# Kernel optimization log

Measured on AMD Instinct MI355X. Metric: run time of the kernel, lower is better.

## Reference

```python
import jax, jax.numpy as jnp
import numpy as np

C = 512
GROUPS = 32
EPS = 1e-5  # torch GroupNorm default


def setup_inputs() -> dict:
    key = jax.random.key(0)
    ks = jax.random.split(key, 11)
    B, H, W = 4, 64, 64
    s = 1.0 / np.sqrt(C)
    inp = {
        "x": jax.random.normal(ks[0], (B, C, H, W), dtype=jnp.float32),
        "gn_scale": jnp.ones((C,), jnp.float32),
        "gn_bias": jnp.zeros((C,), jnp.float32),
        "wq": jax.random.normal(ks[1], (C, C), jnp.float32) * s,
        "bq": jax.random.normal(ks[2], (C,), jnp.float32) * 0.01,
        "wk": jax.random.normal(ks[3], (C, C), jnp.float32) * s,
        "bk": jax.random.normal(ks[4], (C,), jnp.float32) * 0.01,
        "wv": jax.random.normal(ks[5], (C, C), jnp.float32) * s,
        "bv": jax.random.normal(ks[6], (C,), jnp.float32) * 0.01,
        "wo": jax.random.normal(ks[7], (C, C), jnp.float32) * s,
        "bo": jax.random.normal(ks[8], (C,), jnp.float32) * 0.01,
    }
    return inp


def group_norm(x, scale, bias):
    # x: [B, C, H, W]; normalize within each of GROUPS channel groups over (C/G, H, W)
    B, Cc, H, W = x.shape
    xg = x.reshape(B, GROUPS, Cc // GROUPS, H, W)
    mean = jnp.mean(xg, axis=(2, 3, 4), keepdims=True)
    var = jnp.var(xg, axis=(2, 3, 4), keepdims=True)
    xg = (xg - mean) * jax.lax.rsqrt(var + EPS)
    xn = xg.reshape(B, Cc, H, W)
    return xn * scale[None, :, None, None] + bias[None, :, None, None]


def reference(x, gn_scale, gn_bias, wq, bq, wk, bk, wv, bv, wo, bo):
    B, Cc, H, W = x.shape
    h = group_norm(x, gn_scale, gn_bias)
    # 1x1 convs == channel matmuls; work in [B, HW, C] layout
    hf = h.reshape(B, Cc, H * W).transpose(0, 2, 1)  # [B, N, C]
    q = hf @ wq.T + bq                               # [B, N, C]
    k = hf @ wk.T + bk
    v = hf @ wv.T + bv
    scale = jnp.asarray(Cc, x.dtype) ** -0.5
    attn = jnp.einsum("bnc,bmc->bnm", q, k) * scale  # [B, N, N]
    attn = jax.nn.softmax(attn, axis=-1)
    o = jnp.einsum("bnm,bmc->bnc", attn, v)          # [B, N, C]
    o = o @ wo.T + bo
    o = o.transpose(0, 2, 1).reshape(B, Cc, H, W)
    return x + o
```

## Files before the change

kernel.cpp:

```cpp
#include <hip/hip_runtime.h>
#include <cstdint>
#include <cstddef>

typedef unsigned short ushort_t;
typedef __attribute__((ext_vector_type(8))) __bf16 bf16x8;
typedef __attribute__((ext_vector_type(4))) float f32x4;

#define DEVINL __device__ __forceinline__

DEVINL ushort_t f2bf(float f) {
  union { __bf16 b; ushort_t u; } v;
  v.b = (__bf16)f;
  return v.u;
}
DEVINL float bf2f(ushort_t u) {
  union { unsigned u; float f; } v; v.u = ((unsigned)u) << 16;
  return v.f;
}

DEVINL float wred_sum(float x) {
#pragma unroll
  for (int o = 32; o > 0; o >>= 1) x += __shfl_xor(x, o, 64);
  return x;
}

DEVINL void async16(ushort_t* lds, const ushort_t* g) {
  __builtin_amdgcn_global_load_lds(
      (__attribute__((address_space(1))) const unsigned int*)g,
      (__attribute__((address_space(3))) unsigned int*)lds, 16, 0, 0);
}

template <int CPR>
DEVINL int fswz(int r) {
  if constexpr (CPR == 4) return (r >> 2) & 3;
  else return r & 7;
}

__global__ __launch_bounds__(256) void gn_stats_k(const float* __restrict__ x,
                                                  float* __restrict__ stats) {
  const int bg = blockIdx.x;
  const float4* base = (const float4*)(x + ((size_t)bg << 16));
  float s = 0.f, q = 0.f;
  for (int i = threadIdx.x; i < 16384; i += 256) {
    float4 f = base[i];
    s += f.x + f.y + f.z + f.w;
    q += f.x * f.x + f.y * f.y + f.z * f.z + f.w * f.w;
  }
  s = wred_sum(s);
  q = wred_sum(q);
  __shared__ float rs[4], rq[4];
  const int lane = threadIdx.x & 63, wid = threadIdx.x >> 6;
  if (lane == 0) { rs[wid] = s; rq[wid] = q; }
  __syncthreads();
  if (threadIdx.x == 0) {
    float S = rs[0] + rs[1] + rs[2] + rs[3];
    float Q = rq[0] + rq[1] + rq[2] + rq[3];
    float mean = S * (1.f / 65536.f);
    float var = Q * (1.f / 65536.f) - mean * mean;
    stats[2 * bg] = mean;
    stats[2 * bg + 1] = rsqrtf(var + 1e-5f);
  }
}

__global__ __launch_bounds__(256) void gn_apply_k(const float* __restrict__ x,
                                                  const float* __restrict__ stats,
                                                  const float* __restrict__ gs,
                                                  const float* __restrict__ gb,
                                                  ushort_t* __restrict__ h) {
  __shared__ ushort_t tile[32][33];
  const int bid = blockIdx.x;
  const int b = bid >> 11;
  const int r = bid & 2047;
  const int ct = r >> 7, nt = r & 127;
  const int c0 = ct << 5, n0 = nt << 5;
  const int tx = threadIdx.x & 31, ty = threadIdx.x >> 5;
#pragma unroll
  for (int i = 0; i < 4; ++i) {
    const int c = c0 + ty + i * 8;
    const float mean = stats[2 * (b * 32 + (c >> 4))];
    const float rstd = stats[2 * (b * 32 + (c >> 4)) + 1];
    const float xv = x[(((size_t)b * 512 + c) << 12) + n0 + tx];
    tile[ty + i * 8][tx] = f2bf((xv - mean) * rstd * gs[c] + gb[c]);
  }
  __syncthreads();
#pragma unroll
  for (int i = 0; i < 4; ++i) {
    const int n = n0 + ty + i * 8;
    h[(((size_t)b << 12) + n) * 512 + c0 + tx] = tile[tx][ty + i * 8];
  }
}

struct Ptr4 { const float* src[4]; float wsc[4]; };
__global__ __launch_bounds__(256) void cvt_all_k(Ptr4 s, ushort_t* __restrict__ dst) {
  const int i = blockIdx.x * 256 + threadIdx.x;
  const int m = i >> 18;
  dst[i] = f2bf(s.src[m][i & 262143] * s.wsc[m]);
}

struct Ptr3 { const float* bias[3]; ushort_t* out[3]; float bs[3]; };

template <int BM, int BN, int BK, int EPI>
__global__ __launch_bounds__(256) void gemm_nt_k(
    const ushort_t* __restrict__ A, int lda, const ushort_t* __restrict__ Bm, int ldb,
    void* __restrict__ Cout, int ldc, const float* __restrict__ bias,
    const float* __restrict__ resid, float scale, int K,
    size_t azs, size_t bzs, size_t czs, Ptr3 p3) {
  constexpr int CPR = BK / 8;
  constexpr int WTM = BM / 2, WTN = BN / 2;
  constexpr int MI = WTM / 16, NI = WTN / 16;
  constexpr int AR = (BM * CPR) / 256;
  constexpr int BR = (BN * CPR) / 256;
  __shared__ ushort_t Als[BM * BK];
  __shared__ ushort_t Bls[BN * BK];
  const int tid = threadIdx.x;
  const int lane = tid & 63;
  const int wid = tid >> 6;
  const int quad = lane >> 4;
  const int r16 = lane & 15;
  const int wm = wid >> 1, wn = wid & 1;
  const int m0 = blockIdx.y * BM;
  const int n0 = blockIdx.x * BN;
  const int zb = blockIdx.z;

  A += azs * zb;
  Bm += bzs * zb;

  f32x4 acc[MI][NI] = {};

  for (int kt = 0; kt < K; kt += BK) {
#pragma unroll
    for (int r = 0; r < AR; ++r) {
      const int s = r * 256 + tid;
      const int row = s / CPR;
      const int q = (s % CPR) ^ fswz<CPR>(row);
      async16(&Als[s << 3], A + (size_t)(m0 + row) * lda + kt + (q << 3));
    }
#pragma unroll
    for (int r = 0; r < BR; ++r) {
      const int s = r * 256 + tid;
      const int row = s / CPR;
      const int q = (s % CPR) ^ fswz<CPR>(row);
      async16(&Bls[s << 3], Bm + (size_t)(n0 + row) * ldb + kt + (q << 3));
    }
    __syncthreads();
#pragma unroll
    for (int kf = 0; kf < BK / 32; ++kf) {
      bf16x8 af[MI], bfr[NI];
#pragma unroll
      for (int mi = 0; mi < MI; ++mi) {
        const int lr = wm * WTM + mi * 16 + r16;
        const int ch = kf * 4 + quad;
        af[mi] = *reinterpret_cast<const bf16x8*>(
            &Als[(lr * CPR + (ch ^ fswz<CPR>(lr))) << 3]);
      }
#pragma unroll
      for (int ni = 0; ni < NI; ++ni) {
        const int lr = wn * WTN + ni * 16 + r16;
        const int ch = kf * 4 + quad;
        bfr[ni] = *reinterpret_cast<const bf16x8*>(
            &Bls[(lr * CPR + (ch ^ fswz<CPR>(lr))) << 3]);
      }
#pragma unroll
      for (int mi = 0; mi < MI; ++mi)
#pragma unroll
        for (int ni = 0; ni < NI; ++ni)
          acc[mi][ni] = __builtin_amdgcn_mfma_f32_16x16x32_bf16(
              af[mi], bfr[ni], acc[mi][ni], 0, 0, 0);
    }
    __syncthreads();
  }

  const int mrow = m0 + wm * WTM;
  const int ncol = n0 + wn * WTN;
  if constexpr (EPI == 2) {
    float* C = (float*)Cout;
#pragma unroll
    for (int ni = 0; ni < NI; ++ni) {
      const int col = ncol + ni * 16 + r16;
      const float bvv = bias[col];
#pragma unroll
      for (int mi = 0; mi < MI; ++mi) {
        const int rowb = mrow + mi * 16 + quad * 4;
        const int bb = rowb >> 12;
        const int nl = rowb & 4095;
        const size_t base = (((size_t)bb * 512 + col) << 12) + nl;
        const float4 rv = *(const float4*)&resid[base];
        float4 ov;
        ov.x = rv.x + acc[mi][ni][0] + bvv;
        ov.y = rv.y + acc[mi][ni][1] + bvv;
        ov.z = rv.z + acc[mi][ni][2] + bvv;
        ov.w = rv.w + acc[mi][ni][3] + bvv;
        *(float4*)&C[base] = ov;
      }
    }
  } else if constexpr (EPI == 3) {
    const float* bz = p3.bias[zb];
    const float bsc = p3.bs[zb];
    ushort_t* O = p3.out[zb];
    if (zb < 2) {
#pragma unroll
      for (int ni = 0; ni < NI; ++ni) {
        const int col = ncol + ni * 16 + r16;
        const float bvv = bz[col] * bsc;
#pragma unroll
        for (int mi = 0; mi < MI; ++mi) {
          const int rowb = mrow + mi * 16 + quad * 4;
#pragma unroll
          for (int rr = 0; rr < 4; ++rr)
            O[(size_t)(rowb + rr) * 512 + col] = f2bf(acc[mi][ni][rr] + bvv);
        }
      }
    } else {
#pragma unroll
      for (int ni = 0; ni < NI; ++ni) {
        const int col = ncol + ni * 16 + r16;
        const float bvv = bz[col];
#pragma unroll
        for (int mi = 0; mi < MI; ++mi) {
          const int rowb = mrow + mi * 16 + quad * 4;
          const int bb = rowb >> 12;
          const int nn = rowb & 4095;
          ushort4 pk;
          pk.x = f2bf(acc[mi][ni][0] + bvv);
          pk.y = f2bf(acc[mi][ni][1] + bvv);
          pk.z = f2bf(acc[mi][ni][2] + bvv);
          pk.w = f2bf(acc[mi][ni][3] + bvv);
          *(ushort4*)&O[(((size_t)bb * 512 + col) << 12) + nn] = pk;
        }
      }
    }
  }
}

template <int BM, int BN, int WGM, int WGN, int EPI>
__global__ __launch_bounds__(512, 2) void gemm8l_k(
    const ushort_t* __restrict__ A, int lda,
    const ushort_t* __restrict__ Bm, int ldb,
    void* __restrict__ Cout, int ldc, int K,
    size_t azs, size_t bzs, size_t czs) {
  constexpr int WTM = BM / WGM, WTN = BN / WGN;
  constexpr int MI = WTM / 16, NI = WTN / 16;
  constexpr int MH = MI / 2;
  constexpr int ALD = BM / 64;
  constexpr int BLD = BN / 64;
  constexpr int TOT = ALD + BLD;
  constexpr int AHALF = BM * 64;
  constexpr int HALF = (BM + BN) * 64;

  extern __shared__ ushort_t lds8[];
  const int tid = threadIdx.x;
  const int lane = tid & 63;
  const int quad = lane >> 4;
  const int r16 = lane & 15;
  const int wid = tid >> 6;
  const int wm = wid / WGN, wn = wid % WGN;

  int bx, by, bz;
  {
    const int flat = blockIdx.x + (EPI == 4 ? 16 : 4) * (blockIdx.y + 16 * blockIdx.z);
    if constexpr (EPI == 4) {
      const int xcd = flat & 7, s = flat >> 3;
      const int w = s & 31, half = w >> 4, idx = w & 15;
      bx = (xcd & 3) * 4 + (idx & 3);
      by = ((xcd >> 2) + 2 * half) * 4 + (idx >> 2);
      bz = s >> 5;
    } else {
      const int xcd = flat & 7, s = flat >> 3;
      bx = s & 3;
      const int yz = xcd + (s >> 2) * 8;
      by = yz & 15; bz = yz >> 4;
    }
  }
  const int m0 = by * BM, n0 = bx * BN, zb = bz;
  A += azs * zb;
  Bm += bzs * zb;
  const int NT = K >> 6;

  const ushort_t* src[TOT];
  int dsto[TOT];
#pragma unroll
  for (int l = 0; l < TOT; ++l) {
    const bool isA = l < ALD;
    const int li = isA ? l : l - ALD;
    const int s = li * 512 + tid;
    const int row = s >> 3;
    const int q = (s & 7) ^ (row & 7);
    src[l] = (isA ? A + (size_t)(m0 + row) * lda
                  : Bm + (size_t)(n0 + row) * ldb) + (q << 3);
    dsto[l] = (isA ? 0 : AHALF) + (s << 3);
  }

  f32x4 acc[MI][NI] = {};
  f32x4 acc_l[MI] = {};
  bf16x8 ones;
  {
    union { ushort_t u; __bf16 b; } o1; o1.u = 0x3F80;
#pragma unroll
    for (int j = 0; j < 8; ++j) ones[j] = o1.b;
  }

#pragma unroll
  for (int l = 0; l < TOT; ++l) async16(lds8 + dsto[l], src[l]);

  for (int t = 0; t < NT; ++t) {
    const int nbuf = (t + 1) & 1;
    const ushort_t* Ab = lds8 + (t & 1) * HALF;
    const ushort_t* Bb = Ab + AHALF;
    const int koff = ((t + 1 < NT) ? t + 1 : NT - 1) << 6;

    asm volatile("s_waitcnt vmcnt(0) lgkmcnt(0)" ::: "memory");
    __builtin_amdgcn_s_barrier();

#pragma unroll
    for (int l = 0; l < TOT; ++l)
      async16(lds8 + nbuf * HALF + dsto[l], src[l] + koff);

    bf16x8 bfr[NI][2], af[MH][2];
#pragma unroll
    for (int ni = 0; ni < NI; ++ni)
#pragma unroll
      for (int kf = 0; kf < 2; ++kf) {
        const int lr = wn * WTN + ni * 16 + r16;
        const int cc = (kf * 4 + quad) ^ (lr & 7);
        bfr[ni][kf] = *reinterpret_cast<const bf16x8*>(&Bb[lr * 64 + cc * 8]);
      }
#pragma unroll
    for (int h = 0; h < 2; ++h) {
#pragma unroll
      for (int i = 0; i < MH; ++i)
#pragma unroll
        for (int kf = 0; kf < 2; ++kf) {
          const int lr = wm * WTM + (h * MH + i) * 16 + r16;
          const int cc = (kf * 4 + quad) ^ (lr & 7);
          af[i][kf] = *reinterpret_cast<const bf16x8*>(&Ab[lr * 64 + cc * 8]);
        }
      __builtin_amdgcn_s_setprio(1);
#pragma unroll
      for (int i = 0; i < MH; ++i)
#pragma unroll
        for (int ni = 0; ni < NI; ++ni)
#pragma unroll
          for (int kf = 0; kf < 2; ++kf)
            acc[h * MH + i][ni] = __builtin_amdgcn_mfma_f32_16x16x32_bf16(
                af[i][kf], bfr[ni][kf], acc[h * MH + i][ni], 0, 0, 0);
      if constexpr (EPI == 5) {
#pragma unroll
        for (int i = 0; i < MH; ++i)
#pragma unroll
          for (int kf = 0; kf < 2; ++kf)
            acc_l[h * MH + i] = __builtin_amdgcn_mfma_f32_16x16x32_bf16(
                af[i][kf], ones, acc_l[h * MH + i], 0, 0, 0);
      }
      __builtin_amdgcn_s_setprio(0);
    }
  }
  asm volatile("s_waitcnt vmcnt(0)" ::: "memory");

  const int mrow = m0 + wm * WTM;
  const int ncol = n0 + wn * WTN;
  if constexpr (EPI == 4) {
    ushort_t* C = (ushort_t*)Cout + czs * zb;
#pragma unroll
    for (int mi = 0; mi < MI; ++mi) {
#pragma unroll
      for (int rr = 0; rr < 4; ++rr) {
        const int row = mrow + mi * 16 + quad * 4 + rr;
#pragma unroll
        for (int ni = 0; ni < NI; ++ni) {
          const int col = ncol + ni * 16 + r16;
          C[(size_t)row * ldc + col] = f2bf(__expf(acc[mi][ni][rr]));
        }
      }
    }
  } else {
    ushort_t* C = (ushort_t*)Cout + czs * zb;
#pragma unroll
    for (int mi = 0; mi < MI; ++mi) {
#pragma unroll
      for (int rr = 0; rr < 4; ++rr) {
        const int row = mrow + mi * 16 + quad * 4 + rr;
        const float inv = 1.f / acc_l[mi][rr];
#pragma unroll
        for (int ni = 0; ni < NI; ++ni) {
          const int col = ncol + ni * 16 + r16;
          C[(size_t)row * ldc + col] = f2bf(acc[mi][ni][rr] * inv);
        }
      }
    }
  }
}

extern "C" void kernel_launch(void* const* d_in, const int* in_sizes, int n_in,
                              void* d_out, int out_size, void* d_ws, size_t ws_size,
                              hipStream_t stream) {
  const float* x  = (const float*)d_in[0];
  const float* gs = (const float*)d_in[1];
  const float* gb = (const float*)d_in[2];
  const float* wq = (const float*)d_in[3];
  const float* bq = (const float*)d_in[4];
  const float* wk = (const float*)d_in[5];
  const float* bk = (const float*)d_in[6];
  const float* wv = (const float*)d_in[7];
  const float* bv = (const float*)d_in[8];
  const float* wo = (const float*)d_in[9];
  const float* bo = (const float*)d_in[10];
  float* out = (float*)d_out;

  const size_t HNC = (size_t)4 * 4096 * 512;
  char* w = (char*)d_ws;
  float* stats  = (float*)w;    w += 4096;
  ushort_t* wb  = (ushort_t*)w; w += (size_t)4 * 262144 * 2;
  ushort_t* h   = (ushort_t*)w; w += HNC * 2;
  ushort_t* q   = (ushort_t*)w; w += HNC * 2;
  ushort_t* kk  = (ushort_t*)w; w += HNC * 2;
  ushort_t* vt  = (ushort_t*)w; w += HNC * 2;
  ushort_t* Se  = (ushort_t*)w; w += (size_t)4 * 4096 * 4096 * 2;

  const float sc = 0.044194173824159216f;

  static bool attr_done = false;
  if (!attr_done) {
    (void)hipFuncSetAttribute((const void*)gemm8l_k<256, 256, 2, 4, 4>,
                              hipFuncAttributeMaxDynamicSharedMemorySize, 131072);
    (void)hipFuncSetAttribute((const void*)gemm8l_k<256, 128, 4, 2, 5>,
                              hipFuncAttributeMaxDynamicSharedMemorySize, 98304);
    attr_done = true;
  }

  gn_stats_k<<<128, 256, 0, stream>>>(x, stats);
  gn_apply_k<<<8192, 256, 0, stream>>>(x, stats, gs, gb, h);
  Ptr4 wsrc;
  wsrc.src[0] = wq; wsrc.src[1] = wk; wsrc.src[2] = wv; wsrc.src[3] = wo;
  wsrc.wsc[0] = sc; wsrc.wsc[1] = 1.f; wsrc.wsc[2] = 1.f; wsrc.wsc[3] = 1.f;
  cvt_all_k<<<4096, 256, 0, stream>>>(wsrc, wb);

  Ptr3 qkv;
  qkv.bias[0] = bq; qkv.bias[1] = bk; qkv.bias[2] = bv;
  qkv.out[0] = q; qkv.out[1] = kk; qkv.out[2] = vt;
  qkv.bs[0] = sc; qkv.bs[1] = 1.f; qkv.bs[2] = 1.f;
  gemm_nt_k<128, 128, 32, 3><<<dim3(4, 128, 3), 256, 0, stream>>>(
      h, 512, wb, 512, nullptr, 0, nullptr, nullptr, 1.f, 512,
      0, 262144, 0, qkv);

  gemm8l_k<256, 256, 2, 4, 4><<<dim3(16, 16, 4), 512, 131072, stream>>>(
      q, 512, kk, 512, Se, 4096, 512,
      (size_t)4096 * 512, (size_t)4096 * 512, (size_t)4096 * 4096);
  gemm8l_k<256, 128, 4, 2, 5><<<dim3(4, 16, 4), 512, 98304, stream>>>(
      Se, 4096, vt, 4096, h, 512, 4096,
      (size_t)4096 * 4096, (size_t)512 * 4096, (size_t)4096 * 512);

  Ptr3 e0{};
  gemm_nt_k<128, 128, 32, 2><<<dim3(4, 128, 1), 256, 0, stream>>>(
      h, 512, wb + (size_t)3 * 262144, 512, out, 512, bo, x, 1.f, 512,
      0, 0, 0, e0);
}
```

Before: 353.4 us.

## Restructure 8-wave GEMM main loop into barrier-phased LDS-read/MFMA ping-pong schedule

```diff
diff --git a/kernel.cpp b/kernel.cpp
--- a/kernel.cpp
+++ b/kernel.cpp
@@ -233,17 +233,15 @@
 }
 
 template <int BM, int BN, int WGM, int WGN, int EPI>
-__global__ __launch_bounds__(512, 2) void gemm8l_k(
+__global__ __launch_bounds__(512, 2) void gemm8f_k(
     const ushort_t* __restrict__ A, int lda,
     const ushort_t* __restrict__ Bm, int ldb,
     void* __restrict__ Cout, int ldc, int K,
     size_t azs, size_t bzs, size_t czs) {
   constexpr int WTM = BM / WGM, WTN = BN / WGN;
   constexpr int MI = WTM / 16, NI = WTN / 16;
-  constexpr int MH = MI / 2;
-  constexpr int ALD = BM / 64;
-  constexpr int BLD = BN / 64;
-  constexpr int TOT = ALD + BLD;
+  constexpr int MH = MI / 2, NH = NI / 2;
+  constexpr int ALD = BM / 64, BLD = BN / 64, TOT = ALD + BLD;
   constexpr int AHALF = BM * 64;
   constexpr int HALF = (BM + BN) * 64;
 
@@ -301,6 +299,14 @@
 
 #pragma unroll
   for (int l = 0; l < TOT; ++l) async16(lds8 + dsto[l], src[l]);
+  asm volatile("s_waitcnt vmcnt(0)" ::: "memory");
+  __builtin_amdgcn_s_barrier();
+
+#define BARR __builtin_amdgcn_s_barrier()
+#define LGKM0 asm volatile("s_waitcnt lgkmcnt(0)" ::: "memory")
+#define VM0 asm volatile("s_waitcnt vmcnt(0)" ::: "memory")
+#define PRIO1 __builtin_amdgcn_s_setprio(1)
+#define PRIO0 __builtin_amdgcn_s_setprio(0)
 
   for (int t = 0; t < NT; ++t) {
     const int nbuf = (t + 1) & 1;
@@ -308,53 +314,116 @@
     const ushort_t* Bb = Ab + AHALF;
     const int koff = ((t + 1 < NT) ? t + 1 : NT - 1) << 6;
 
-    asm volatile("s_waitcnt vmcnt(0) lgkmcnt(0)" ::: "memory");
-    __builtin_amdgcn_s_barrier();
-
-#pragma unroll
-    for (int l = 0; l < TOT; ++l)
+#define S_RDA(h)                                                               \
+    _Pragma("unroll") for (int i = 0; i < MH; ++i)                             \
+    _Pragma("unroll") for (int kf = 0; kf < 2; ++kf) {                         \
+      const int lr = wm * WTM + ((h) * MH + i) * 16 + r16;                     \
+      const int cc = (kf * 4 + quad) ^ (lr & 7);                               \
+      a_[i][kf] = *reinterpret_cast<const bf16x8*>(&Ab[lr * 64 + cc * 8]); }
+#define S_RDB(dst, h)                                                          \
+    _Pragma("unroll") for (int j = 0; j < NH; ++j)                             \
+    _Pragma("unroll") for (int kf = 0; kf < 2; ++kf) {                         \
+      const int lr = wn * WTN + ((h) * NH + j) * 16 + r16;                     \
+      const int cc = (kf * 4 + quad) ^ (lr & 7);                               \
+      dst[j][kf] = *reinterpret_cast<const bf16x8*>(&Bb[lr * 64 + cc * 8]); }
+#define S_MMA(mh, bsrc, nh)                                                    \
+    PRIO1;                                                                     \
+    _Pragma("unroll") for (int i = 0; i < MH; ++i)                             \
+    _Pragma("unroll") for (int j = 0; j < NH; ++j)                             \
+    _Pragma("unroll") for (int kf = 0; kf < 2; ++kf)                           \
+      acc[(mh) * MH + i][(nh) * NH + j] =                                      \
+          __builtin_amdgcn_mfma_f32_16x16x32_bf16(                             \
+              a_[i][kf], bsrc[j][kf], acc[(mh) * MH + i][(nh) * NH + j],       \
+              0, 0, 0);                                                        \
+    PRIO0;
+#define STAGE_ALL                                                              \
+    _Pragma("unroll")                                                          \
+    for (int l = 0; l < TOT; ++l)                                              \
       async16(lds8 + nbuf * HALF + dsto[l], src[l] + koff);
 
-    bf16x8 bfr[NI][2], af[MH][2];
-#pragma unroll
-    for (int ni = 0; ni < NI; ++ni)
-#pragma unroll
-      for (int kf = 0; kf < 2; ++kf) {
-        const int lr = wn * WTN + ni * 16 + r16;
-        const int cc = (kf * 4 + quad) ^ (lr & 7);
-        bfr[ni][kf] = *reinterpret_cast<const bf16x8*>(&Bb[lr * 64 + cc * 8]);
-      }
-#pragma unroll
-    for (int h = 0; h < 2; ++h) {
+    if constexpr (EPI == 4) {
+      bf16x8 a_[MH][2], b0_[NH][2], b1_[NH][2];
+      S_RDA(0) S_RDB(b0_, 0)
+      STAGE_ALL
+      BARR; LGKM0;
+      S_MMA(0, b0_, 0)
+      BARR;
+      S_RDB(b1_, 1)
+      BARR; LGKM0;
+      S_MMA(0, b1_, 1)
+      BARR;
+      S_RDA(1)
+      BARR; LGKM0;
+      S_MMA(1, b1_, 1)
+      BARR;
+      S_RDB(b0_, 0)
+      BARR; LGKM0;
+      S_MMA(1, b0_, 0)
+      VM0;
+      BARR;
+    } else {
+      bf16x8 a_[MH][2], b_[NI][2];
+      S_RDA(0)
+#pragma unroll
+      for (int j = 0; j < NI; ++j)
+#pragma unroll
+        for (int kf = 0; kf < 2; ++kf) {
+          const int lr = wn * WTN + j * 16 + r16;
+          const int cc = (kf * 4 + quad) ^ (lr & 7);
+          b_[j][kf] = *reinterpret_cast<const bf16x8*>(&Bb[lr * 64 + cc * 8]);
+        }
+      STAGE_ALL
+      BARR; LGKM0;
+      PRIO1;
 #pragma unroll
       for (int i = 0; i < MH; ++i)
 #pragma unroll
-        for (int kf = 0; kf < 2; ++kf) {
-          const int lr = wm * WTM + (h * MH + i) * 16 + r16;
-          const int cc = (kf * 4 + quad) ^ (lr & 7);
-          af[i][kf] = *reinterpret_cast<const bf16x8*>(&Ab[lr * 64 + cc * 8]);
-        }
-      __builtin_amdgcn_s_setprio(1);
+        for (int j = 0; j < NI; ++j)
+#pragma unroll
+          for (int kf = 0; kf < 2; ++kf)
+            acc[i][j] = __builtin_amdgcn_mfma_f32_16x16x32_bf16(
+                a_[i][kf], b_[j][kf], acc[i][j], 0, 0, 0);
 #pragma unroll
       for (int i = 0; i < MH; ++i)
 #pragma unroll
-        for (int ni = 0; ni < NI; ++ni)
+        for (int kf = 0; kf < 2; ++kf)
+          acc_l[i] = __builtin_amdgcn_mfma_f32_16x16x32_bf16(
+              a_[i][kf], ones, acc_l[i], 0, 0, 0);
+      PRIO0;
+      BARR;
+      S_RDA(1)
+      BARR; LGKM0;
+      PRIO1;
+#pragma unroll
+      for (int i = 0; i < MH; ++i)
+#pragma unroll
+        for (int j = 0; j < NI; ++j)
 #pragma unroll
           for (int kf = 0; kf < 2; ++kf)
-            acc[h * MH + i][ni] = __builtin_amdgcn_mfma_f32_16x16x32_bf16(
-                af[i][kf], bfr[ni][kf], acc[h * MH + i][ni], 0, 0, 0);
-      if constexpr (EPI == 5) {
-#pragma unroll
-        for (int i = 0; i < MH; ++i)
-#pragma unroll
-          for (int kf = 0; kf < 2; ++kf)
-            acc_l[h * MH + i] = __builtin_amdgcn_mfma_f32_16x16x32_bf16(
-                af[i][kf], ones, acc_l[h * MH + i], 0, 0, 0);
-      }
-      __builtin_amdgcn_s_setprio(0);
-    }
-  }
-  asm volatile("s_waitcnt vmcnt(0)" ::: "memory");
+            acc[MH + i][j] = __builtin_amdgcn_mfma_f32_16x16x32_bf16(
+                a_[i][kf], b_[j][kf], acc[MH + i][j], 0, 0, 0);
+#pragma unroll
+      for (int i = 0; i < MH; ++i)
+#pragma unroll
+        for (int kf = 0; kf < 2; ++kf)
+          acc_l[MH + i] = __builtin_amdgcn_mfma_f32_16x16x32_bf16(
+              a_[i][kf], ones, acc_l[MH + i], 0, 0, 0);
+      PRIO0;
+      VM0;
+      BARR;
+    }
+#undef S_RDA
+#undef S_RDB
+#undef S_MMA
+#undef STAGE_ALL
+  }
+  VM0;
+
+#undef BARR
+#undef LGKM0
+#undef VM0
+#undef PRIO1
+#undef PRIO0
 
   const int mrow = m0 + wm * WTM;
   const int ncol = n0 + wn * WTN;
@@ -420,9 +489,9 @@
 
   static bool attr_done = false;
   if (!attr_done) {
-    (void)hipFuncSetAttribute((const void*)gemm8l_k<256, 256, 2, 4, 4>,
+    (void)hipFuncSetAttribute((const void*)gemm8f_k<256, 256, 2, 4, 4>,
                               hipFuncAttributeMaxDynamicSharedMemorySize, 131072);
-    (void)hipFuncSetAttribute((const void*)gemm8l_k<256, 128, 4, 2, 5>,
+    (void)hipFuncSetAttribute((const void*)gemm8f_k<256, 128, 4, 2, 5>,
                               hipFuncAttributeMaxDynamicSharedMemorySize, 98304);
     attr_done = true;
   }
@@ -442,10 +511,10 @@
       h, 512, wb, 512, nullptr, 0, nullptr, nullptr, 1.f, 512,
       0, 262144, 0, qkv);
 
-  gemm8l_k<256, 256, 2, 4, 4><<<dim3(16, 16, 4), 512, 131072, stream>>>(
+  gemm8f_k<256, 256, 2, 4, 4><<<dim3(16, 16, 4), 512, 131072, stream>>>(
       q, 512, kk, 512, Se, 4096, 512,
       (size_t)4096 * 512, (size_t)4096 * 512, (size_t)4096 * 4096);
-  gemm8l_k<256, 128, 4, 2, 5><<<dim3(4, 16, 4), 512, 98304, stream>>>(
+  gemm8f_k<256, 128, 4, 2, 5><<<dim3(4, 16, 4), 512, 98304, stream>>>(
       Se, 4096, vt, 4096, h, 512, 4096,
       (size_t)4096 * 4096, (size_t)512 * 4096, (size_t)4096 * 512);
 
```

Result: slower. 365.9 us (+3.6%).

## Route QKV and output projections through pipelined 8-wave GEMM, split GN stats

Applied to the files above, without the earlier changes.

```diff
diff --git a/kernel.cpp b/kernel.cpp
--- a/kernel.cpp
+++ b/kernel.cpp
@@ -38,10 +38,10 @@
 
 __global__ __launch_bounds__(256) void gn_stats_k(const float* __restrict__ x,
                                                   float* __restrict__ stats) {
-  const int bg = blockIdx.x;
-  const float4* base = (const float4*)(x + ((size_t)bg << 16));
+  const int bg = blockIdx.x >> 2, sl = blockIdx.x & 3;
+  const float4* base = (const float4*)(x + ((size_t)bg << 16) + (sl << 14));
   float s = 0.f, q = 0.f;
-  for (int i = threadIdx.x; i < 16384; i += 256) {
+  for (int i = threadIdx.x; i < 4096; i += 256) {
     float4 f = base[i];
     s += f.x + f.y + f.z + f.w;
     q += f.x * f.x + f.y * f.y + f.z * f.z + f.w * f.w;
@@ -53,12 +53,8 @@
   if (lane == 0) { rs[wid] = s; rq[wid] = q; }
   __syncthreads();
   if (threadIdx.x == 0) {
-    float S = rs[0] + rs[1] + rs[2] + rs[3];
-    float Q = rq[0] + rq[1] + rq[2] + rq[3];
-    float mean = S * (1.f / 65536.f);
-    float var = Q * (1.f / 65536.f) - mean * mean;
-    stats[2 * bg] = mean;
-    stats[2 * bg + 1] = rsqrtf(var + 1e-5f);
+    atomicAdd(&stats[2 * bg], rs[0] + rs[1] + rs[2] + rs[3]);
+    atomicAdd(&stats[2 * bg + 1], rq[0] + rq[1] + rq[2] + rq[3]);
   }
 }
 
@@ -77,8 +73,10 @@
 #pragma unroll
   for (int i = 0; i < 4; ++i) {
     const int c = c0 + ty + i * 8;
-    const float mean = stats[2 * (b * 32 + (c >> 4))];
-    const float rstd = stats[2 * (b * 32 + (c >> 4)) + 1];
+    const int gidx = b * 32 + (c >> 4);
+    const float mean = stats[2 * gidx] * (1.f / 65536.f);
+    const float var = stats[2 * gidx + 1] * (1.f / 65536.f) - mean * mean;
+    const float rstd = rsqrtf(var + 1e-5f);
     const float xv = x[(((size_t)b * 512 + c) << 12) + n0 + tx];
     tile[ty + i * 8][tx] = f2bf((xv - mean) * rstd * gs[c] + gb[c]);
   }
@@ -99,80 +97,162 @@
 
 struct Ptr3 { const float* bias[3]; ushort_t* out[3]; float bs[3]; };
 
-template <int BM, int BN, int BK, int EPI>
-__global__ __launch_bounds__(256) void gemm_nt_k(
-    const ushort_t* __restrict__ A, int lda, const ushort_t* __restrict__ Bm, int ldb,
-    void* __restrict__ Cout, int ldc, const float* __restrict__ bias,
-    const float* __restrict__ resid, float scale, int K,
-    size_t azs, size_t bzs, size_t czs, Ptr3 p3) {
-  constexpr int CPR = BK / 8;
-  constexpr int WTM = BM / 2, WTN = BN / 2;
+template <int BM, int BN, int WGM, int WGN, int EPI>
+__global__ __launch_bounds__(512, 2) void gemm8l_k(
+    const ushort_t* __restrict__ A, int lda,
+    const ushort_t* __restrict__ Bm, int ldb,
+    void* __restrict__ Cout, int ldc, int K,
+    size_t azs, size_t bzs, size_t czs,
+    const float* __restrict__ bias, const float* __restrict__ resid, Ptr3 p3) {
+  constexpr int WTM = BM / WGM, WTN = BN / WGN;
   constexpr int MI = WTM / 16, NI = WTN / 16;
-  constexpr int AR = (BM * CPR) / 256;
-  constexpr int BR = (BN * CPR) / 256;
-  __shared__ ushort_t Als[BM * BK];
-  __shared__ ushort_t Bls[BN * BK];
+  constexpr int MH = MI / 2;
+  constexpr int ALD = BM / 64, BLD = BN / 64, TOT = ALD + BLD;
+  constexpr int AHALF = BM * 64;
+  constexpr int HALF = (BM + BN) * 64;
+
+  extern __shared__ ushort_t lds8[];
   const int tid = threadIdx.x;
   const int lane = tid & 63;
-  const int wid = tid >> 6;
   const int quad = lane >> 4;
   const int r16 = lane & 15;
-  const int wm = wid >> 1, wn = wid & 1;
-  const int m0 = blockIdx.y * BM;
-  const int n0 = blockIdx.x * BN;
-  const int zb = blockIdx.z;
-
+  const int wid = tid >> 6;
+  const int wm = wid / WGN, wn = wid % WGN;
+
+  int bx, by, bz;
+  if constexpr (EPI == 4) {
+    const int flat = blockIdx.x + 16 * (blockIdx.y + 16 * blockIdx.z);
+    const int xcd = flat & 7, s = flat >> 3;
+    const int w = s & 31, half = w >> 4, idx = w & 15;
+    bx = (xcd & 3) * 4 + (idx & 3);
+    by = ((xcd >> 2) + 2 * half) * 4 + (idx >> 2);
+    bz = s >> 5;
+  } else if constexpr (EPI == 5) {
+    const int flat = blockIdx.x + 4 * (blockIdx.y + 16 * blockIdx.z);
+    const int xcd = flat & 7, s = flat >> 3;
+    bx = s & 3;
+    const int yz = xcd + (s >> 2) * 8;
+    by = yz & 15; bz = yz >> 4;
+  } else {
+    bx = blockIdx.x; by = blockIdx.y; bz = blockIdx.z;
+  }
+  const int m0 = by * BM, n0 = bx * BN, zb = bz;
   A += azs * zb;
   Bm += bzs * zb;
+  const int NT = K >> 6;
+
+  const ushort_t* src[TOT];
+  int dsto[TOT];
+#pragma unroll
+  for (int l = 0; l < TOT; ++l) {
+    const bool isA = l < ALD;
+    const int li = isA ? l : l - ALD;
+    const int s = li * 512 + tid;
+    const int row = s >> 3;
+    const int q = (s & 7) ^ (row & 7);
+    src[l] = (isA ? A + (size_t)(m0 + row) * lda
+                  : Bm + (size_t)(n0 + row) * ldb) + (q << 3);
+    dsto[l] = (isA ? 0 : AHALF) + (s << 3);
+  }
 
   f32x4 acc[MI][NI] = {};
-
-  for (int kt = 0; kt < K; kt += BK) {
-#pragma unroll
-    for (int r = 0; r < AR; ++r) {
-      const int s = r * 256 + tid;
-      const int row = s / CPR;
-      const int q = (s % CPR) ^ fswz<CPR>(row);
-      async16(&Als[s << 3], A + (size_t)(m0 + row) * lda + kt + (q << 3));
-    }
-#pragma unroll
-    for (int r = 0; r < BR; ++r) {
-      const int s = r * 256 + tid;
-      const int row = s / CPR;
-      const int q = (s % CPR) ^ fswz<CPR>(row);
-      async16(&Bls[s << 3], Bm + (size_t)(n0 + row) * ldb + kt + (q << 3));
-    }
-    __syncthreads();
-#pragma unroll
-    for (int kf = 0; kf < BK / 32; ++kf) {
-      bf16x8 af[MI], bfr[NI];
-#pragma unroll
-      for (int mi = 0; mi < MI; ++mi) {
-        const int lr = wm * WTM + mi * 16 + r16;
-        const int ch = kf * 4 + quad;
-        af[mi] = *reinterpret_cast<const bf16x8*>(
-            &Als[(lr * CPR + (ch ^ fswz<CPR>(lr))) << 3]);
-      }
-#pragma unroll
-      for (int ni = 0; ni < NI; ++ni) {
+  f32x4 acc_l[MI] = {};
+  bf16x8 ones;
+  {
+    union { ushort_t u; __bf16 b; } o1; o1.u = 0x3F80;
+#pragma unroll
+    for (int j = 0; j < 8; ++j) ones[j] = o1.b;
+  }
+
+#pragma unroll
+  for (int l = 0; l < TOT; ++l) async16(lds8 + dsto[l], src[l]);
+
+  for (int t = 0; t < NT; ++t) {
+    const int nbuf = (t + 1) & 1;
+    const ushort_t* Ab = lds8 + (t & 1) * HALF;
+    const ushort_t* Bb = Ab + AHALF;
+    const int koff = ((t + 1 < NT) ? t + 1 : NT - 1) << 6;
+
+    asm volatile("s_waitcnt vmcnt(0) lgkmcnt(0)" ::: "memory");
+    __builtin_amdgcn_s_barrier();
+
+#pragma unroll
+    for (int l = 0; l < TOT; ++l)
+      async16(lds8 + nbuf * HALF + dsto[l], src[l] + koff);
+
+    bf16x8 bfr[NI][2], af[MH][2];
+#pragma unroll
+    for (int ni = 0; ni < NI; ++ni)
+#pragma unroll
+      for (int kf = 0; kf < 2; ++kf) {
         const int lr = wn * WTN + ni * 16 + r16;
-        const int ch = kf * 4 + quad;
-        bfr[ni] = *reinterpret_cast<const bf16x8*>(
-            &Bls[(lr * CPR + (ch ^ fswz<CPR>(lr))) << 3]);
-      }
-#pragma unroll
-      for (int mi = 0; mi < MI; ++mi)
+        const int cc = (kf * 4 + quad) ^ (lr & 7);
+        bfr[ni][kf] = *reinterpret_cast<const bf16x8*>(&Bb[lr * 64 + cc * 8]);
+      }
+#pragma unroll
+    for (int h = 0; h < 2; ++h) {
+#pragma unroll
+      for (int i = 0; i < MH; ++i)
+#pragma unroll
+        for (int kf = 0; kf < 2; ++kf) {
+          const int lr = wm * WTM + (h * MH + i) * 16 + r16;
+          const int cc = (kf * 4 + quad) ^ (lr & 7);
+          af[i][kf] = *reinterpret_cast<const bf16x8*>(&Ab[lr * 64 + cc * 8]);
+        }
+      __builtin_amdgcn_s_setprio(1);
+#pragma unroll
+      for (int i = 0; i < MH; ++i)
 #pragma unroll
         for (int ni = 0; ni < NI; ++ni)
-          acc[mi][ni] = __builtin_amdgcn_mfma_f32_16x16x32_bf16(
-              af[mi], bfr[ni], acc[mi][ni], 0, 0, 0);
-    }
-    __syncthreads();
-  }
+#pragma unroll
+          for (int kf = 0; kf < 2; ++kf)
+            acc[h * MH + i][ni] = __builtin_amdgcn_mfma_f32_16x16x32_bf16(
+                af[i][kf], bfr[ni][kf], acc[h * MH + i][ni], 0, 0, 0);
+      if constexpr (EPI == 5) {
+#pragma unroll
+        for (int i = 0; i < MH; ++i)
+#pragma unroll
+          for (int kf = 0; kf < 2; ++kf)
+            acc_l[h * MH + i] = __builtin_amdgcn_mfma_f32_16x16x32_bf16(
+                af[i][kf], ones, acc_l[h * MH + i], 0, 0, 0);
+      }
+      __builtin_amdgcn_s_setprio(0);
+    }
+  }
+  asm volatile("s_waitcnt vmcnt(0)" ::: "memory");
 
   const int mrow = m0 + wm * WTM;
   const int ncol = n0 + wn * WTN;
-  if constexpr (EPI == 2) {
+  if constexpr (EPI == 4) {
+    ushort_t* C = (ushort_t*)Cout + czs * zb;
+#pragma unroll
+    for (int mi = 0; mi < MI; ++mi) {
+#pragma unroll
+      for (int rr = 0; rr < 4; ++rr) {
+        const int row = mrow + mi * 16 + quad * 4 + rr;
+#pragma unroll
+        for (int ni = 0; ni < NI; ++ni) {
+          const int col = ncol + ni * 16 + r16;
+          C[(size_t)row * ldc + col] = f2bf(__expf(acc[mi][ni][rr]));
+        }
+      }
+    }
+  } else if constexpr (EPI == 5) {
+    ushort_t* C = (ushort_t*)Cout + czs * zb;
+#pragma unroll
+    for (int mi = 0; mi < MI; ++mi) {
+#pragma unroll
+      for (int rr = 0; rr < 4; ++rr) {
+        const int row = mrow + mi * 16 + quad * 4 + rr;
+        const float inv = 1.f / acc_l[mi][rr];
+#pragma unroll
+        for (int ni = 0; ni < NI; ++ni) {
+          const int col = ncol + ni * 16 + r16;
+          C[(size_t)row * ldc + col] = f2bf(acc[mi][ni][rr] * inv);
+        }
+      }
+    }
+  } else if constexpr (EPI == 2) {
     float* C = (float*)Cout;
 #pragma unroll
     for (int ni = 0; ni < NI; ++ni) {
@@ -193,7 +273,7 @@
         *(float4*)&C[base] = ov;
       }
     }
-  } else if constexpr (EPI == 3) {
+  } else {
     const float* bz = p3.bias[zb];
     const float bsc = p3.bs[zb];
     ushort_t* O = p3.out[zb];
@@ -226,164 +306,6 @@
           pk.z = f2bf(acc[mi][ni][2] + bvv);
           pk.w = f2bf(acc[mi][ni][3] + bvv);
           *(ushort4*)&O[(((size_t)bb * 512 + col) << 12) + nn] = pk;
-        }
-      }
-    }
-  }
-}
-
-template <int BM, int BN, int WGM, int WGN, int EPI>
-__global__ __launch_bounds__(512, 2) void gemm8l_k(
-    const ushort_t* __restrict__ A, int lda,
-    const ushort_t* __restrict__ Bm, int ldb,
-    void* __restrict__ Cout, int ldc, int K,
-    size_t azs, size_t bzs, size_t czs) {
-  constexpr int WTM = BM / WGM, WTN = BN / WGN;
-  constexpr int MI = WTM / 16, NI = WTN / 16;
-  constexpr int MH = MI / 2;
-  constexpr int ALD = BM / 64;
-  constexpr int BLD = BN / 64;
-  constexpr int TOT = ALD + BLD;
-  constexpr int AHALF = BM * 64;
-  constexpr int HALF = (BM + BN) * 64;
-
-  extern __shared__ ushort_t lds8[];
-  const int tid = threadIdx.x;
-  const int lane = tid & 63;
-  const int quad = lane >> 4;
-  const int r16 = lane & 15;
-  const int wid = tid >> 6;
-  const int wm = wid / WGN, wn = wid % WGN;
-
-  int bx, by, bz;
-  {
-    const int flat = blockIdx.x + (EPI == 4 ? 16 : 4) * (blockIdx.y + 16 * blockIdx.z);
-    if constexpr (EPI == 4) {
-      const int xcd = flat & 7, s = flat >> 3;
-      const int w = s & 31, half = w >> 4, idx = w & 15;
-      bx = (xcd & 3) * 4 + (idx & 3);
-      by = ((xcd >> 2) + 2 * half) * 4 + (idx >> 2);
-      bz = s >> 5;
-    } else {
-      const int xcd = flat & 7, s = flat >> 3;
-      bx = s & 3;
-      const int yz = xcd + (s >> 2) * 8;
-      by = yz & 15; bz = yz >> 4;
-    }
-  }
-  const int m0 = by * BM, n0 = bx * BN, zb = bz;
-  A += azs * zb;
-  Bm += bzs * zb;
-  const int NT = K >> 6;
-
-  const ushort_t* src[TOT];
-  int dsto[TOT];
-#pragma unroll
-  for (int l = 0; l < TOT; ++l) {
-    const bool isA = l < ALD;
-    const int li = isA ? l : l - ALD;
-    const int s = li * 512 + tid;
-    const int row = s >> 3;
-    const int q = (s & 7) ^ (row & 7);
-    src[l] = (isA ? A + (size_t)(m0 + row) * lda
-                  : Bm + (size_t)(n0 + row) * ldb) + (q << 3);
-    dsto[l] = (isA ? 0 : AHALF) + (s << 3);
-  }
-
-  f32x4 acc[MI][NI] = {};
-  f32x4 acc_l[MI] = {};
-  bf16x8 ones;
-  {
-    union { ushort_t u; __bf16 b; } o1; o1.u = 0x3F80;
-#pragma unroll
-    for (int j = 0; j < 8; ++j) ones[j] = o1.b;
-  }
-
-#pragma unroll
-  for (int l = 0; l < TOT; ++l) async16(lds8 + dsto[l], src[l]);
-
-  for (int t = 0; t < NT; ++t) {
-    const int nbuf = (t + 1) & 1;
-    const ushort_t* Ab = lds8 + (t & 1) * HALF;
-    const ushort_t* Bb = Ab + AHALF;
-    const int koff = ((t + 1 < NT) ? t + 1 : NT - 1) << 6;
-
-    asm volatile("s_waitcnt vmcnt(0) lgkmcnt(0)" ::: "memory");
-    __builtin_amdgcn_s_barrier();
-
-#pragma unroll
-    for (int l = 0; l < TOT; ++l)
-      async16(lds8 + nbuf * HALF + dsto[l], src[l] + koff);
-
-    bf16x8 bfr[NI][2], af[MH][2];
-#pragma unroll
-    for (int ni = 0; ni < NI; ++ni)
-#pragma unroll
-      for (int kf = 0; kf < 2; ++kf) {
-        const int lr = wn * WTN + ni * 16 + r16;
-        const int cc = (kf * 4 + quad) ^ (lr & 7);
-        bfr[ni][kf] = *reinterpret_cast<const bf16x8*>(&Bb[lr * 64 + cc * 8]);
-      }
-#pragma unroll
-    for (int h = 0; h < 2; ++h) {
-#pragma unroll
-      for (int i = 0; i < MH; ++i)
-#pragma unroll
-        for (int kf = 0; kf < 2; ++kf) {
-          const int lr = wm * WTM + (h * MH + i) * 16 + r16;
-          const int cc = (kf * 4 + quad) ^ (lr & 7);
-          af[i][kf] = *reinterpret_cast<const bf16x8*>(&Ab[lr * 64 + cc * 8]);
-        }
-      __builtin_amdgcn_s_setprio(1);
-#pragma unroll
-      for (int i = 0; i < MH; ++i)
-#pragma unroll
-        for (int ni = 0; ni < NI; ++ni)
-#pragma unroll
-          for (int kf = 0; kf < 2; ++kf)
-            acc[h * MH + i][ni] = __builtin_amdgcn_mfma_f32_16x16x32_bf16(
-                af[i][kf], bfr[ni][kf], acc[h * MH + i][ni], 0, 0, 0);
-      if constexpr (EPI == 5) {
-#pragma unroll
-        for (int i = 0; i < MH; ++i)
-#pragma unroll
-          for (int kf = 0; kf < 2; ++kf)
-            acc_l[h * MH + i] = __builtin_amdgcn_mfma_f32_16x16x32_bf16(
-                af[i][kf], ones, acc_l[h * MH + i], 0, 0, 0);
-      }
-      __builtin_amdgcn_s_setprio(0);
-    }
-  }
-  asm volatile("s_waitcnt vmcnt(0)" ::: "memory");
-
-  const int mrow = m0 + wm * WTM;
-  const int ncol = n0 + wn * WTN;
-  if constexpr (EPI == 4) {
-    ushort_t* C = (ushort_t*)Cout + czs * zb;
-#pragma unroll
-    for (int mi = 0; mi < MI; ++mi) {
-#pragma unroll
-      for (int rr = 0; rr < 4; ++rr) {
-        const int row = mrow + mi * 16 + quad * 4 + rr;
-#pragma unroll
-        for (int ni = 0; ni < NI; ++ni) {
-          const int col = ncol + ni * 16 + r16;
-          C[(size_t)row * ldc + col] = f2bf(__expf(acc[mi][ni][rr]));
-        }
-      }
-    }
-  } else {
-    ushort_t* C = (ushort_t*)Cout + czs * zb;
-#pragma unroll
-    for (int mi = 0; mi < MI; ++mi) {
-#pragma unroll
-      for (int rr = 0; rr < 4; ++rr) {
-        const int row = mrow + mi * 16 + quad * 4 + rr;
-        const float inv = 1.f / acc_l[mi][rr];
-#pragma unroll
-        for (int ni = 0; ni < NI; ++ni) {
-          const int col = ncol + ni * 16 + r16;
-          C[(size_t)row * ldc + col] = f2bf(acc[mi][ni][rr] * inv);
         }
       }
     }
@@ -424,10 +346,15 @@
                               hipFuncAttributeMaxDynamicSharedMemorySize, 131072);
     (void)hipFuncSetAttribute((const void*)gemm8l_k<256, 128, 4, 2, 5>,
                               hipFuncAttributeMaxDynamicSharedMemorySize, 98304);
+    (void)hipFuncSetAttribute((const void*)gemm8l_k<256, 128, 4, 2, 3>,
+                              hipFuncAttributeMaxDynamicSharedMemorySize, 98304);
+    (void)hipFuncSetAttribute((const void*)gemm8l_k<256, 128, 4, 2, 2>,
+                              hipFuncAttributeMaxDynamicSharedMemorySize, 98304);
     attr_done = true;
   }
 
-  gn_stats_k<<<128, 256, 0, stream>>>(x, stats);
+  hipMemsetAsync(stats, 0, 128 * 2 * sizeof(float), stream);
+  gn_stats_k<<<512, 256, 0, stream>>>(x, stats);
   gn_apply_k<<<8192, 256, 0, stream>>>(x, stats, gs, gb, h);
   Ptr4 wsrc;
   wsrc.src[0] = wq; wsrc.src[1] = wk; wsrc.src[2] = wv; wsrc.src[3] = wo;
@@ -438,19 +365,22 @@
   qkv.bias[0] = bq; qkv.bias[1] = bk; qkv.bias[2] = bv;
   qkv.out[0] = q; qkv.out[1] = kk; qkv.out[2] = vt;
   qkv.bs[0] = sc; qkv.bs[1] = 1.f; qkv.bs[2] = 1.f;
-  gemm_nt_k<128, 128, 32, 3><<<dim3(4, 128, 3), 256, 0, stream>>>(
-      h, 512, wb, 512, nullptr, 0, nullptr, nullptr, 1.f, 512,
-      0, 262144, 0, qkv);
+  Ptr3 e0{};
+
+  gemm8l_k<256, 128, 4, 2, 3><<<dim3(4, 64, 3), 512, 98304, stream>>>(
+      h, 512, wb, 512, nullptr, 512, 512,
+      0, 262144, 0, nullptr, nullptr, qkv);
 
   gemm8l_k<256, 256, 2, 4, 4><<<dim3(16, 16, 4), 512, 131072, stream>>>(
       q, 512, kk, 512, Se, 4096, 512,
-      (size_t)4096 * 512, (size_t)4096 * 512, (size_t)4096 * 4096);
+      (size_t)4096 * 512, (size_t)4096 * 512, (size_t)4096 * 4096,
+      nullptr, nullptr, e0);
   gemm8l_k<256, 128, 4, 2, 5><<<dim3(4, 16, 4), 512, 98304, stream>>>(
       Se, 4096, vt, 4096, h, 512, 4096,
-      (size_t)4096 * 4096, (size_t)512 * 4096, (size_t)4096 * 512);
-
-  Ptr3 e0{};
-  gemm_nt_k<128, 128, 32, 2><<<dim3(4, 128, 1), 256, 0, stream>>>(
-      h, 512, wb + (size_t)3 * 262144, 512, out, 512, bo, x, 1.f, 512,
-      0, 0, 0, e0);
-}
+      (size_t)4096 * 4096, (size_t)512 * 4096, (size_t)4096 * 512,
+      nullptr, nullptr, e0);
+
+  gemm8l_k<256, 128, 4, 2, 2><<<dim3(4, 64, 1), 512, 98304, stream>>>(
+      h, 512, wb + (size_t)3 * 262144, 512, out, 512, 512,
+      0, 0, 0, bo, x, e0);
+}
```

Result: faster. 336.4 us (-4.8%).
